# Performance work log

Measured on AMD Instinct MI355X. Metric: run time of the kernel, lower is better.

## Reference

```python
import jax, jax.numpy as jnp
import numpy as np

D_IN = 768
D_OUT = 768
SEQ = 2048
BATCH = 4


def setup_inputs() -> dict:
    key = jax.random.key(0)
    kx, kq, kk, kv = jax.random.split(key, 4)
    # torch Linear weight shape: [d_out, d_in]; default init ~ U(-1/sqrt(d_in), 1/sqrt(d_in))
    bound = 1.0 / np.sqrt(D_IN)
    x = jax.random.normal(kx, (BATCH, SEQ, D_IN), dtype=jnp.float32)
    Wq = jax.random.uniform(kq, (D_OUT, D_IN), jnp.float32, -bound, bound)
    Wk = jax.random.uniform(kk, (D_OUT, D_IN), jnp.float32, -bound, bound)
    Wv = jax.random.uniform(kv, (D_OUT, D_IN), jnp.float32, -bound, bound)
    return {"x": x, "Wq": Wq, "Wk": Wk, "Wv": Wv}


def reference(x, Wq, Wk, Wv):
    # QKV projections (no bias): x [b, n, d_in] @ W.T -> [b, n, d_out]
    q = jnp.einsum("bnd,od->bno", x, Wq)
    k = jnp.einsum("bnd,od->bno", x, Wk)
    v = jnp.einsum("bnd,od->bno", x, Wv)
    n = x.shape[1]
    d_k = k.shape[-1]
    # scores [b, n, n]; causal mask: positions j > i set to -inf
    scores = jnp.einsum("bqd,bkd->bqk", q, k)
    causal = jnp.triu(jnp.ones((n, n), dtype=bool), k=1)  # True above diagonal
    scores = jnp.where(causal[None, :, :], -jnp.inf, scores)
    attn = jax.nn.softmax(scores / jnp.sqrt(jnp.asarray(d_k, scores.dtype)), axis=-1)
    # dropout p=0.0 -> identity
    context = jnp.einsum("bqk,bkd->bqd", attn, v)
    return context
```

## Files before the change

kernel.cpp:

```cpp
#include <hip/hip_runtime.h>
#include <hip/hip_bf16.h>

typedef float f32x4 __attribute__((ext_vector_type(4)));
typedef short s16x8 __attribute__((ext_vector_type(8)));

#define B_ 4
#define S_ 2048
#define D_ 768

typedef const __attribute__((address_space(1))) char* gas_t;
typedef __attribute__((address_space(3))) char* las_t;

__device__ __forceinline__ void gload_lds16(const void* g, void* l) {
  __builtin_amdgcn_global_load_lds((gas_t)g, (las_t)l, 16, 0, 0);
}

__global__ void cvt_kernel(const float* __restrict__ x,
                           const float* __restrict__ wq,
                           const float* __restrict__ wk,
                           const float* __restrict__ wv,
                           __hip_bfloat16* __restrict__ xb,
                           __hip_bfloat16* __restrict__ wqb,
                           __hip_bfloat16* __restrict__ wkb,
                           __hip_bfloat16* __restrict__ wvb) {
  const int NX = B_ * S_ * D_ / 4;
  const int NW = D_ * D_ / 4;
  int stride = gridDim.x * blockDim.x;
  for (int j = blockIdx.x * blockDim.x + threadIdx.x; j < NX + 3 * NW; j += stride) {
    const float4* src; __hip_bfloat16* dst; int off;
    if (j < NX)             { src = (const float4*)x;  dst = xb;  off = j; }
    else if (j < NX + NW)   { src = (const float4*)wq; dst = wqb; off = j - NX; }
    else if (j < NX + 2*NW) { src = (const float4*)wk; dst = wkb; off = j - NX - NW; }
    else                    { src = (const float4*)wv; dst = wvb; off = j - NX - 2*NW; }
    float4 v = src[off];
    dst[4*off+0] = __float2bfloat16(v.x);
    dst[4*off+1] = __float2bfloat16(v.y);
    dst[4*off+2] = __float2bfloat16(v.z);
    dst[4*off+3] = __float2bfloat16(v.w);
  }
}

__device__ __forceinline__ void stage_tile64(const __hip_bfloat16* __restrict__ base,
                                             size_t stride, int r0, int k0,
                                             char* lds, int w, int l) {
#pragma unroll
  for (int it = 0; it < 4; ++it) {
    int ra = it * 32 + w * 8 + (l >> 3);
    int ca = (l & 7) * 8;
    gload_lds16(base + (size_t)(r0 + ra) * stride + k0 + ca,
                lds + it * 4096 + w * 1024);
  }
}

__launch_bounds__(256, 4)
__global__ void qkv_gemm(const __hip_bfloat16* __restrict__ xb,
                         const __hip_bfloat16* __restrict__ wqb,
                         const __hip_bfloat16* __restrict__ wkb,
                         const __hip_bfloat16* __restrict__ wvb,
                         __hip_bfloat16* __restrict__ Qb,
                         __hip_bfloat16* __restrict__ Kb,
                         __hip_bfloat16* __restrict__ Vt) {
  __shared__ __hip_bfloat16 At[128 * 64];
  __shared__ __hip_bfloat16 Bt[128 * 64];
  const int z = blockIdx.z;
  const __hip_bfloat16* Ag;
  const __hip_bfloat16* Bg;
  int m0, n0;
  if (z == 0)      { Ag = xb;  Bg = wqb; m0 = blockIdx.x * 128; n0 = blockIdx.y * 128; }
  else if (z == 1) { Ag = xb;  Bg = wkb; m0 = blockIdx.x * 128; n0 = blockIdx.y * 128; }
  else             { Ag = wvb; Bg = xb;  m0 = blockIdx.y * 128; n0 = blockIdx.x * 128; }

  const int tid = threadIdx.x, w = tid >> 6, l = tid & 63;
  const int wr = w >> 1, wc = w & 1;
  f32x4 acc[4][4] = {};

  for (int k0 = 0; k0 < 768; k0 += 64) {
    __syncthreads();
    stage_tile64(Ag, 768, m0, k0, (char*)At, w, l);
    stage_tile64(Bg, 768, n0, k0, (char*)Bt, w, l);
    __syncthreads();
#pragma unroll
    for (int kk = 0; kk < 2; ++kk) {
      s16x8 a[4], b[4];
#pragma unroll
      for (int i = 0; i < 4; ++i) {
        a[i] = *(const s16x8*)&At[(wr * 64 + i * 16 + (l & 15)) * 64 + kk * 32 + (l >> 4) * 8];
        b[i] = *(const s16x8*)&Bt[(wc * 64 + i * 16 + (l & 15)) * 64 + kk * 32 + (l >> 4) * 8];
      }
#pragma unroll
      for (int i = 0; i < 4; ++i)
#pragma unroll
        for (int j = 0; j < 4; ++j)
          acc[i][j] = __builtin_amdgcn_mfma_f32_16x16x32_bf16(a[i], b[j], acc[i][j], 0, 0, 0);
    }
  }

  if (z < 2) {
    __hip_bfloat16* outp = (z == 0) ? Qb : Kb;
#pragma unroll
    for (int i = 0; i < 4; ++i) {
      int m = m0 + wr * 64 + i * 16 + (l >> 4) * 4;
#pragma unroll
      for (int j = 0; j < 4; ++j) {
        int n = n0 + wc * 64 + j * 16 + (l & 15);
#pragma unroll
        for (int r = 0; r < 4; ++r)
          outp[(size_t)(m + r) * 768 + n] = __float2bfloat16(acc[i][j][r]);
      }
    }
  } else {
#pragma unroll
    for (int i = 0; i < 4; ++i) {
      int dd = m0 + wr * 64 + i * 16 + (l >> 4) * 4;
#pragma unroll
      for (int j = 0; j < 4; ++j) {
        int sg = n0 + wc * 64 + j * 16 + (l & 15);
        int bb = sg >> 11, sl = sg & 2047;
#pragma unroll
        for (int r = 0; r < 4; ++r)
          Vt[(size_t)bb * D_ * S_ + (size_t)(dd + r) * S_ + sl] = __float2bfloat16(acc[i][j][r]);
      }
    }
  }
}

__launch_bounds__(256, 4)
__global__ void qk_gemm(const __hip_bfloat16* __restrict__ Qb,
                        const __hip_bfloat16* __restrict__ Kb,
                        __hip_bfloat16* __restrict__ Sb) {
  __shared__ __hip_bfloat16 At[128 * 64];
  __shared__ __hip_bfloat16 Bt[128 * 64];
  const int qt = blockIdx.x, kt = blockIdx.y, b = blockIdx.z;
  if (kt > qt) return;
  const int m0 = qt * 128, n0 = kt * 128;
  const __hip_bfloat16* Ag = Qb + (size_t)b * S_ * D_;
  const __hip_bfloat16* Bg = Kb + (size_t)b * S_ * D_;
  const int tid = threadIdx.x, w = tid >> 6, l = tid & 63;
  const int wr = w >> 1, wc = w & 1;
  const float SC = 0.03608439182435161f * 1.4426950408889634f;
  f32x4 acc[4][4] = {};

  for (int k0 = 0; k0 < D_; k0 += 64) {
    __syncthreads();
    stage_tile64(Ag, D_, m0, k0, (char*)At, w, l);
    stage_tile64(Bg, D_, n0, k0, (char*)Bt, w, l);
    __syncthreads();
#pragma unroll
    for (int kk = 0; kk < 2; ++kk) {
      s16x8 a[4], bfr[4];
#pragma unroll
      for (int i = 0; i < 4; ++i) {
        a[i]   = *(const s16x8*)&At[(wr * 64 + i * 16 + (l & 15)) * 64 + kk * 32 + (l >> 4) * 8];
        bfr[i] = *(const s16x8*)&Bt[(wc * 64 + i * 16 + (l & 15)) * 64 + kk * 32 + (l >> 4) * 8];
      }
#pragma unroll
      for (int i = 0; i < 4; ++i)
#pragma unroll
        for (int j = 0; j < 4; ++j)
          acc[i][j] = __builtin_amdgcn_mfma_f32_16x16x32_bf16(a[i], bfr[j], acc[i][j], 0, 0, 0);
    }
  }

#pragma unroll
  for (int i = 0; i < 4; ++i) {
    int m = m0 + wr * 64 + i * 16 + (l >> 4) * 4;
#pragma unroll
    for (int j = 0; j < 4; ++j) {
      int n = n0 + wc * 64 + j * 16 + (l & 15);
#pragma unroll
      for (int r = 0; r < 4; ++r) {
        float zz = (n > m + r) ? -1e30f : acc[i][j][r] * SC;
        Sb[(size_t)(b * S_ + m + r) * S_ + n] = __float2bfloat16(zz);
      }
    }
  }
}

__launch_bounds__(256, 4)
__global__ void softmax_kernel(const __hip_bfloat16* __restrict__ Sb,
                               __hip_bfloat16* __restrict__ Pb) {
  const int tid = threadIdx.x, w = tid >> 6, l = tid & 63;
  const int r = blockIdx.x * 4 + w;
  const int q = r & (S_ - 1);
  const int L = ((q >> 7) + 1) << 7;
  const ushort* srow = (const ushort*)(Sb + (size_t)r * S_);
  ushort* prow = (ushort*)(Pb + (size_t)r * S_);
  f32x4 ch[8];
#pragma unroll
  for (int it = 0; it < 8; ++it) {
    int idx = it * 256 + l * 4;
    if (idx < L) {
      ushort4 u = *(const ushort4*)&srow[idx];
      ch[it].x = __uint_as_float((unsigned)u.x << 16);
      ch[it].y = __uint_as_float((unsigned)u.y << 16);
      ch[it].z = __uint_as_float((unsigned)u.z << 16);
      ch[it].w = __uint_as_float((unsigned)u.w << 16);
    } else {
      ch[it].x = -1e30f; ch[it].y = -1e30f; ch[it].z = -1e30f; ch[it].w = -1e30f;
    }
  }
  float mx = -1e30f;
#pragma unroll
  for (int it = 0; it < 8; ++it)
    mx = fmaxf(mx, fmaxf(fmaxf(ch[it].x, ch[it].y), fmaxf(ch[it].z, ch[it].w)));
#pragma unroll
  for (int d = 1; d < 64; d <<= 1) mx = fmaxf(mx, __shfl_xor(mx, d, 64));
  float sum = 0.f;
#pragma unroll
  for (int it = 0; it < 8; ++it) {
    ch[it].x = exp2f(ch[it].x - mx);
    ch[it].y = exp2f(ch[it].y - mx);
    ch[it].z = exp2f(ch[it].z - mx);
    ch[it].w = exp2f(ch[it].w - mx);
    sum += (ch[it].x + ch[it].y) + (ch[it].z + ch[it].w);
  }
#pragma unroll
  for (int d = 1; d < 64; d <<= 1) sum += __shfl_xor(sum, d, 64);
  const float rinv = 1.0f / sum;
#pragma unroll
  for (int it = 0; it < 8; ++it) {
    int idx = it * 256 + l * 4;
    if (idx < L) {
      __hip_bfloat16 h0 = __float2bfloat16(ch[it].x * rinv);
      __hip_bfloat16 h1 = __float2bfloat16(ch[it].y * rinv);
      __hip_bfloat16 h2 = __float2bfloat16(ch[it].z * rinv);
      __hip_bfloat16 h3 = __float2bfloat16(ch[it].w * rinv);
      ushort4 u;
      u.x = *(ushort*)&h0; u.y = *(ushort*)&h1; u.z = *(ushort*)&h2; u.w = *(ushort*)&h3;
      *(ushort4*)&prow[idx] = u;
    }
  }
}

__launch_bounds__(256, 4)
__global__ void pv_gemm(const __hip_bfloat16* __restrict__ Pb,
                        const __hip_bfloat16* __restrict__ Vt,
                        float* __restrict__ out) {
  __shared__ __hip_bfloat16 At[128 * 64];
  __shared__ __hip_bfloat16 Bt[128 * 64];
  const int qt = 15 - (int)blockIdx.x, dt = blockIdx.y, b = blockIdx.z;
  const int m0 = qt * 128, n0 = dt * 128;
  const __hip_bfloat16* Ag = Pb + (size_t)b * S_ * S_;
  const __hip_bfloat16* Bg = Vt + (size_t)b * D_ * S_;
  const int tid = threadIdx.x, w = tid >> 6, l = tid & 63;
  const int wr = w >> 1, wc = w & 1;
  const int kmax = (qt + 1) * 128;
  f32x4 acc[4][4] = {};

  for (int k0 = 0; k0 < kmax; k0 += 64) {
    __syncthreads();
    stage_tile64(Ag, S_, m0, k0, (char*)At, w, l);
    stage_tile64(Bg, S_, n0, k0, (char*)Bt, w, l);
    __syncthreads();
#pragma unroll
    for (int kk = 0; kk < 2; ++kk) {
      s16x8 a[4], bfr[4];
#pragma unroll
      for (int i = 0; i < 4; ++i) {
        a[i]   = *(const s16x8*)&At[(wr * 64 + i * 16 + (l & 15)) * 64 + kk * 32 + (l >> 4) * 8];
        bfr[i] = *(const s16x8*)&Bt[(wc * 64 + i * 16 + (l & 15)) * 64 + kk * 32 + (l >> 4) * 8];
      }
#pragma unroll
      for (int i = 0; i < 4; ++i)
#pragma unroll
        for (int j = 0; j < 4; ++j)
          acc[i][j] = __builtin_amdgcn_mfma_f32_16x16x32_bf16(a[i], bfr[j], acc[i][j], 0, 0, 0);
    }
  }

#pragma unroll
  for (int i = 0; i < 4; ++i) {
    int m = m0 + wr * 64 + i * 16 + (l >> 4) * 4;
#pragma unroll
    for (int j = 0; j < 4; ++j) {
      int n = n0 + wc * 64 + j * 16 + (l & 15);
#pragma unroll
      for (int r = 0; r < 4; ++r)
        out[(size_t)(b * S_ + m + r) * D_ + n] = acc[i][j][r];
    }
  }
}

extern "C" void kernel_launch(void* const* d_in, const int* in_sizes, int n_in,
                              void* d_out, int out_size, void* d_ws, size_t ws_size,
                              hipStream_t stream) {
  const float* x  = (const float*)d_in[0];
  const float* wq = (const float*)d_in[1];
  const float* wk = (const float*)d_in[2];
  const float* wv = (const float*)d_in[3];
  char* ws = (char*)d_ws;
  __hip_bfloat16* xb  = (__hip_bfloat16*)(ws + 0);
  __hip_bfloat16* wqb = (__hip_bfloat16*)(ws + 12582912);
  __hip_bfloat16* wkb = (__hip_bfloat16*)(ws + 12582912 + 1179648);
  __hip_bfloat16* wvb = (__hip_bfloat16*)(ws + 12582912 + 2 * 1179648);
  __hip_bfloat16* Qb  = (__hip_bfloat16*)(ws + 16121856);
  __hip_bfloat16* Kb  = (__hip_bfloat16*)(ws + 28704768);
  __hip_bfloat16* Vt  = (__hip_bfloat16*)(ws + 41287680);
  __hip_bfloat16* Sb  = (__hip_bfloat16*)(ws + 53870592);
  __hip_bfloat16* Pb  = (__hip_bfloat16*)(ws + 0);

  cvt_kernel<<<2048, 256, 0, stream>>>(x, wq, wk, wv, xb, wqb, wkb, wvb);
  qkv_gemm<<<dim3(64, 6, 3), 256, 0, stream>>>(xb, wqb, wkb, wvb, Qb, Kb, Vt);
  qk_gemm<<<dim3(16, 16, 4), 256, 0, stream>>>(Qb, Kb, Sb);
  softmax_kernel<<<2048, 256, 0, stream>>>(Sb, Pb);
  pv_gemm<<<dim3(16, 6, 4), 256, 0, stream>>>(Pb, Vt, (float*)d_out);
}
```

Measured before the change: 222.9 us.

## Double-buffer LDS tiles with prefetch and XOR-swizzle LDS layout in GEMMs

The three GEMM kernels (QKV projection, QK^T, PV) now keep two LDS buffers per operand. The next K-tile is prefetched with global_load_lds while MFMAs run on the current tile, which removes one barrier per iteration and hides global load latency. The 16-byte column slots are also XOR-swizzled by row within each 64-wide tile, to cut LDS bank conflicts on the fragment reads. The cost is doubled shared memory per block (64 KB), so the launch bounds drop from 4 to 2 blocks per CU, which lowers occupancy.

```diff
diff --git a/kernel.cpp b/kernel.cpp
--- a/kernel.cpp
+++ b/kernel.cpp
@@ -46,13 +46,15 @@
 #pragma unroll
   for (int it = 0; it < 4; ++it) {
     int ra = it * 32 + w * 8 + (l >> 3);
-    int ca = (l & 7) * 8;
-    gload_lds16(base + (size_t)(r0 + ra) * stride + k0 + ca,
+    int slot = (l & 7) ^ ((l >> 3) & 7);
+    gload_lds16(base + (size_t)(r0 + ra) * stride + k0 + slot * 8,
                 lds + it * 4096 + w * 1024);
   }
 }
 
-__launch_bounds__(256, 4)
+#define SWZ_IDX(R, s) ((R) * 64 + (((s) ^ ((R) & 7)) * 8))
+
+__launch_bounds__(256, 2)
 __global__ void qkv_gemm(const __hip_bfloat16* __restrict__ xb,
                          const __hip_bfloat16* __restrict__ wqb,
                          const __hip_bfloat16* __restrict__ wkb,
@@ -60,8 +62,8 @@
                          __hip_bfloat16* __restrict__ Qb,
                          __hip_bfloat16* __restrict__ Kb,
                          __hip_bfloat16* __restrict__ Vt) {
-  __shared__ __hip_bfloat16 At[128 * 64];
-  __shared__ __hip_bfloat16 Bt[128 * 64];
+  __shared__ __hip_bfloat16 At[2][128 * 64];
+  __shared__ __hip_bfloat16 Bt[2][128 * 64];
   const int z = blockIdx.z;
   const __hip_bfloat16* Ag;
   const __hip_bfloat16* Bg;
@@ -74,18 +76,25 @@
   const int wr = w >> 1, wc = w & 1;
   f32x4 acc[4][4] = {};
 
+  stage_tile64(Ag, 768, m0, 0, (char*)At[0], w, l);
+  stage_tile64(Bg, 768, n0, 0, (char*)Bt[0], w, l);
+  int cur = 0;
   for (int k0 = 0; k0 < 768; k0 += 64) {
     __syncthreads();
-    stage_tile64(Ag, 768, m0, k0, (char*)At, w, l);
-    stage_tile64(Bg, 768, n0, k0, (char*)Bt, w, l);
-    __syncthreads();
+    if (k0 + 64 < 768) {
+      stage_tile64(Ag, 768, m0, k0 + 64, (char*)At[cur ^ 1], w, l);
+      stage_tile64(Bg, 768, n0, k0 + 64, (char*)Bt[cur ^ 1], w, l);
+    }
 #pragma unroll
     for (int kk = 0; kk < 2; ++kk) {
       s16x8 a[4], b[4];
+      int s = kk * 4 + (l >> 4);
 #pragma unroll
       for (int i = 0; i < 4; ++i) {
-        a[i] = *(const s16x8*)&At[(wr * 64 + i * 16 + (l & 15)) * 64 + kk * 32 + (l >> 4) * 8];
-        b[i] = *(const s16x8*)&Bt[(wc * 64 + i * 16 + (l & 15)) * 64 + kk * 32 + (l >> 4) * 8];
+        int Ra = wr * 64 + i * 16 + (l & 15);
+        int Rb = wc * 64 + i * 16 + (l & 15);
+        a[i] = *(const s16x8*)&At[cur][SWZ_IDX(Ra, s)];
+        b[i] = *(const s16x8*)&Bt[cur][SWZ_IDX(Rb, s)];
       }
 #pragma unroll
       for (int i = 0; i < 4; ++i)
@@ -93,6 +102,7 @@
         for (int j = 0; j < 4; ++j)
           acc[i][j] = __builtin_amdgcn_mfma_f32_16x16x32_bf16(a[i], b[j], acc[i][j], 0, 0, 0);
     }
+    cur ^= 1;
   }
 
   if (z < 2) {
@@ -124,12 +134,12 @@
   }
 }
 
-__launch_bounds__(256, 4)
+__launch_bounds__(256, 2)
 __global__ void qk_gemm(const __hip_bfloat16* __restrict__ Qb,
                         const __hip_bfloat16* __restrict__ Kb,
                         __hip_bfloat16* __restrict__ Sb) {
-  __shared__ __hip_bfloat16 At[128 * 64];
-  __shared__ __hip_bfloat16 Bt[128 * 64];
+  __shared__ __hip_bfloat16 At[2][128 * 64];
+  __shared__ __hip_bfloat16 Bt[2][128 * 64];
   const int qt = blockIdx.x, kt = blockIdx.y, b = blockIdx.z;
   if (kt > qt) return;
   const int m0 = qt * 128, n0 = kt * 128;
@@ -140,18 +150,25 @@
   const float SC = 0.03608439182435161f * 1.4426950408889634f;
   f32x4 acc[4][4] = {};
 
+  stage_tile64(Ag, D_, m0, 0, (char*)At[0], w, l);
+  stage_tile64(Bg, D_, n0, 0, (char*)Bt[0], w, l);
+  int cur = 0;
   for (int k0 = 0; k0 < D_; k0 += 64) {
     __syncthreads();
-    stage_tile64(Ag, D_, m0, k0, (char*)At, w, l);
-    stage_tile64(Bg, D_, n0, k0, (char*)Bt, w, l);
-    __syncthreads();
+    if (k0 + 64 < D_) {
+      stage_tile64(Ag, D_, m0, k0 + 64, (char*)At[cur ^ 1], w, l);
+      stage_tile64(Bg, D_, n0, k0 + 64, (char*)Bt[cur ^ 1], w, l);
+    }
 #pragma unroll
     for (int kk = 0; kk < 2; ++kk) {
       s16x8 a[4], bfr[4];
+      int s = kk * 4 + (l >> 4);
 #pragma unroll
       for (int i = 0; i < 4; ++i) {
-        a[i]   = *(const s16x8*)&At[(wr * 64 + i * 16 + (l & 15)) * 64 + kk * 32 + (l >> 4) * 8];
-        bfr[i] = *(const s16x8*)&Bt[(wc * 64 + i * 16 + (l & 15)) * 64 + kk * 32 + (l >> 4) * 8];
+        int Ra = wr * 64 + i * 16 + (l & 15);
+        int Rb = wc * 64 + i * 16 + (l & 15);
+        a[i]   = *(const s16x8*)&At[cur][SWZ_IDX(Ra, s)];
+        bfr[i] = *(const s16x8*)&Bt[cur][SWZ_IDX(Rb, s)];
       }
 #pragma unroll
       for (int i = 0; i < 4; ++i)
@@ -159,6 +176,7 @@
         for (int j = 0; j < 4; ++j)
           acc[i][j] = __builtin_amdgcn_mfma_f32_16x16x32_bf16(a[i], bfr[j], acc[i][j], 0, 0, 0);
     }
+    cur ^= 1;
   }
 
 #pragma unroll
@@ -232,12 +250,12 @@
   }
 }
 
-__launch_bounds__(256, 4)
+__launch_bounds__(256, 2)
 __global__ void pv_gemm(const __hip_bfloat16* __restrict__ Pb,
                         const __hip_bfloat16* __restrict__ Vt,
                         float* __restrict__ out) {
-  __shared__ __hip_bfloat16 At[128 * 64];
-  __shared__ __hip_bfloat16 Bt[128 * 64];
+  __shared__ __hip_bfloat16 At[2][128 * 64];
+  __shared__ __hip_bfloat16 Bt[2][128 * 64];
   const int qt = 15 - (int)blockIdx.x, dt = blockIdx.y, b = blockIdx.z;
   const int m0 = qt * 128, n0 = dt * 128;
   const __hip_bfloat16* Ag = Pb + (size_t)b * S_ * S_;
@@ -247,18 +265,25 @@
   const int kmax = (qt + 1) * 128;
   f32x4 acc[4][4] = {};
 
+  stage_tile64(Ag, S_, m0, 0, (char*)At[0], w, l);
+  stage_tile64(Bg, S_, n0, 0, (char*)Bt[0], w, l);
+  int cur = 0;
   for (int k0 = 0; k0 < kmax; k0 += 64) {
     __syncthreads();
-    stage_tile64(Ag, S_, m0, k0, (char*)At, w, l);
-    stage_tile64(Bg, S_, n0, k0, (char*)Bt, w, l);
-    __syncthreads();
+    if (k0 + 64 < kmax) {
+      stage_tile64(Ag, S_, m0, k0 + 64, (char*)At[cur ^ 1], w, l);
+      stage_tile64(Bg, S_, n0, k0 + 64, (char*)Bt[cur ^ 1], w, l);
+    }
 #pragma unroll
     for (int kk = 0; kk < 2; ++kk) {
       s16x8 a[4], bfr[4];
+      int s = kk * 4 + (l >> 4);
 #pragma unroll
       for (int i = 0; i < 4; ++i) {
-        a[i]   = *(const s16x8*)&At[(wr * 64 + i * 16 + (l & 15)) * 64 + kk * 32 + (l >> 4) * 8];
-        bfr[i] = *(const s16x8*)&Bt[(wc * 64 + i * 16 + (l & 15)) * 64 + kk * 32 + (l >> 4) * 8];
+        int Ra = wr * 64 + i * 16 + (l & 15);
+        int Rb = wc * 64 + i * 16 + (l & 15);
+        a[i]   = *(const s16x8*)&At[cur][SWZ_IDX(Ra, s)];
+        bfr[i] = *(const s16x8*)&Bt[cur][SWZ_IDX(Rb, s)];
       }
 #pragma unroll
       for (int i = 0; i < 4; ++i)
@@ -266,6 +291,7 @@
         for (int j = 0; j < 4; ++j)
           acc[i][j] = __builtin_amdgcn_mfma_f32_16x16x32_bf16(a[i], bfr[j], acc[i][j], 0, 0, 0);
     }
+    cur ^= 1;
   }
 
 #pragma unroll
```

Result: faster. 196.4 us (-11.9%).
